# Optimization experiments

Measured on AMD Instinct MI355X. Metric: run time of the kernel, lower is better.

The kernel has to match this reference:

```python
import jax, jax.numpy as jnp
import numpy as np

N = 20000      # nodes
L = 64         # seq_length
E = 64         # emb_size
V = 30000      # vocab_size
HG = 128       # gnn_hidden_size
HT = 128       # text_hidden_size
NE = 640000    # edges
EPS = 1e-12


def _normalize(x):
    # F.normalize(x, p=2, dim=1) on [N, E, L]
    n = jnp.sqrt(jnp.sum(x * x, axis=1, keepdims=True))
    return x / jnp.maximum(n, EPS)


def gcn_conv(x, W, b, src_idx, dst_idx, n_nodes):
    # PyG GCNConv: add self-loops, symmetric normalization D^-1/2 (A+I) D^-1/2 (X W) + b
    h = x @ W                                            # [N, out]
    deg = jnp.zeros((n_nodes,), h.dtype).at[dst_idx].add(1.0) + 1.0  # incl. self-loop
    dinv = jax.lax.rsqrt(deg)
    norm = dinv[src_idx] * dinv[dst_idx]                 # [NE]
    msg = h[src_idx] * norm[:, None]                     # gather + scale
    out = jnp.zeros_like(h).at[dst_idx].add(msg)         # scatter-add to targets
    out = out + h * (dinv * dinv)[:, None]               # self-loop term
    return out + b


def setup_inputs() -> dict:
    key = jax.random.key(0)
    ks = jax.random.split(key, 12)
    rn = lambda k, shape: jax.random.normal(k, shape, jnp.float32) * 0.02
    return {
        "src": jax.random.randint(ks[0], (N, L), 0, V),
        "seg": jax.random.randint(ks[1], (N, L), 0, 3),
        "edge_index": jax.random.randint(ks[2], (2, NE), 0, N),
        "src_emb": rn(ks[3], (V, E)),
        "seg_emb": rn(ks[4], (3, E)),
        "w": jnp.ones((L,), jnp.float32),
        "Wq1": rn(ks[5], (E, HT)), "bq1": jnp.zeros((HT,), jnp.float32),
        "Wq2": rn(ks[6], (HT, E)), "bq2": jnp.zeros((E,), jnp.float32),
        "Wg1": rn(ks[7], (E, HG)), "bg1": jnp.zeros((HG,), jnp.float32),
        "Wg2": rn(ks[8], (HG, E)), "bg2": jnp.zeros((E,), jnp.float32),
        "Wl": rn(ks[9], (E, E)),   "bl": jnp.zeros((E,), jnp.float32),
    }


def reference(src, seg, edge_index, src_emb, seg_emb, w, Wq1, bq1, Wq2, bq2,
              Wg1, bg1, Wg2, bg2, Wl, bl):
    # --- LiteratureEmbedding ---
    se = src_emb[src]                 # [N, L, E]
    ge = seg_emb[seg]                 # [N, L, E]
    sv = se.reshape(-1, E, L)         # raw view (matches torch .view, not transpose)
    gv = ge.reshape(-1, E, L)
    f = (_normalize(w * sv) + _normalize(gv)).sum(-1)   # [N, E]
    # --- query MLP ---
    x = jax.nn.relu(f @ Wq1 + bq1) @ Wq2 + bq2
    # --- two GCN layers ---
    si, di = edge_index[0], edge_index[1]
    x = jax.nn.relu(gcn_conv(x, Wg1, bg1, si, di, N))
    x = jax.nn.relu(gcn_conv(x, Wg2, bg2, si, di, N))
    # --- output linear (dropout is identity in eval) ---
    return x @ Wl + bl
```

## Files before the change

### kernel.cpp

```cpp
#include <hip/hip_runtime.h>

#if defined(__has_builtin)
#if __has_builtin(__builtin_amdgcn_readlane)
#define READLANE(v, l) __builtin_amdgcn_readlane((v), (l))
#else
#define READLANE(v, l) __shfl((v), (l))
#endif
#else
#define READLANE(v, l) __shfl((v), (l))
#endif
__device__ __forceinline__ float readlane_f(float v, int l) {
    return __uint_as_float(READLANE(__float_as_uint(v), l));
}

__device__ __forceinline__ unsigned short f2bf(float x) {
    unsigned u = __float_as_uint(x);
    u += 0x7FFFu + ((u >> 16) & 1u);
    return (unsigned short)(u >> 16);
}

#define CAPLOG 8

__global__ __launch_bounds__(256) void prep0_k(
    const float* __restrict__ src_emb, unsigned short* __restrict__ sbf, int ve,
    int* __restrict__ cursor, int n,
    unsigned* __restrict__ Cz, unsigned* __restrict__ Az, int convB)
{
    const int b = blockIdx.x, t = threadIdx.x;
    if (b < convB) {
        int i = (b * 256 + t) * 4;
        if (i + 3 < ve) {
            float4 v = *(const float4*)&src_emb[i];
            ushort4 u;
            u.x = f2bf(v.x); u.y = f2bf(v.y); u.z = f2bf(v.z); u.w = f2bf(v.w);
            *(ushort4*)&sbf[i] = u;
        } else {
            for (; i < ve; ++i) sbf[i] = f2bf(src_emb[i]);
        }
    } else {
        int i = (b - convB) * 256 + t;
        if (i < n) cursor[i] = 0;
        if (b == convB && t < 32) { Cz[t] = 0u; Az[t] = 0u; }
    }
}

__global__ __launch_bounds__(256) void prep1_k(
    const int* __restrict__ si, const int* __restrict__ di,
    int* __restrict__ cursor, int* __restrict__ edge_off, int ne, int eB,
    const int* __restrict__ src, const int* __restrict__ seg,
    const unsigned short* __restrict__ sbf, const float* __restrict__ seg_emb,
    const float* __restrict__ wvec, float* __restrict__ f)
{
    const int t = threadIdx.x;
    if ((int)blockIdx.x < eB) {
        int i = blockIdx.x * 256 + t;
        if (i < ne) {
            int d = di[i];
            int pos = atomicAdd(cursor + d, 1);
            edge_off[((long)d << CAPLOG) + pos] = si[i] << 7;
        }
        return;
    }
    __shared__ __align__(16) float S[64 * 65];
    __shared__ float red[4][64];
    __shared__ float part2[4][64];
    __shared__ float coef[64];
    __shared__ float rGs[64];
    __shared__ float segE[192];
    __shared__ float dG[3];
    __shared__ int   gidxS[64];
    __shared__ int   cnt3[3];

    const int wid = t >> 6, q = t & 63;
    const long n = blockIdx.x - eB;

    if (wid == 0) {
        int c = seg[n * 64 + q];
        gidxS[q] = c;
        unsigned long long b0 = __ballot(c == 0);
        unsigned long long b1 = __ballot(c == 1);
        if (q == 0) {
            int n0 = __popcll(b0), n1 = __popcll(b1);
            cnt3[0] = n0; cnt3[1] = n1; cnt3[2] = 64 - n0 - n1;
        }
    } else if (t < 64 + 192) {
        segE[t - 64] = seg_emb[t - 64];
    }

    const int p0 = wid * 16;
    int off = src[n * 64 + p0 + (q & 15)] << 7;
    const char* base = (const char*)sbf;
    const int q2 = q << 1;
    float s2 = 0.f;
    #pragma unroll
    for (int pp = 0; pp < 16; ++pp) {
        int so = READLANE(off, pp);
        unsigned short u = *(const unsigned short*)(base + (so + q2));
        float v = __uint_as_float((unsigned)u << 16);
        S[(p0 + pp) * 65 + q] = v;
        s2 += v * v;
    }
    red[wid][q] = s2;
    __syncthreads();

    if (t < 64) {
        float ts = red[0][t] + red[1][t] + red[2][t] + red[3][t];
        float wq = wvec[t];
        coef[t] = wq / fmaxf(fabsf(wq) * sqrtf(ts), 1e-12f);
        float e0 = segE[t], e1 = segE[64 + t], e2 = segE[128 + t];
        float g2 = (float)cnt3[0] * e0 * e0 + (float)cnt3[1] * e1 * e1
                 + (float)cnt3[2] * e2 * e2;
        rGs[t] = 1.f / fmaxf(sqrtf(g2), 1e-12f);
    }
    __syncthreads();

    if (t < 3) {
        float a = 0.f;
        for (int k = 0; k < 64; ++k) a += segE[t * 64 + k] * rGs[k];
        dG[t] = a;
    }
    float acc = 0.f;
    const int k0 = wid * 16;
    #pragma unroll
    for (int kk = 0; kk < 16; ++kk)
        acc += S[q * 65 + k0 + kk] * coef[k0 + kk];
    part2[wid][q] = acc;
    __syncthreads();

    if (t < 64)
        f[n * 64 + t] = part2[0][t] + part2[1][t] + part2[2][t] + part2[3][t]
                        + dG[gidxS[t]];
}

__device__ __forceinline__ float4 csr_gather4_bf(const char* __restrict__ hb,
                                                 const int* __restrict__ eo,
                                                 int dn, int j, int zoff)
{
    const int grp = j >> 4;
    const int col = (j & 15) << 3;
    float4 a0 = make_float4(0.f, 0.f, 0.f, 0.f);
    float4 a1 = a0, a2 = a0, a3 = a0;
#define ACC(d, a)                                                        \
    { a.x += __uint_as_float((d).x << 16);                               \
      a.y += __uint_as_float((d).x & 0xFFFF0000u);                       \
      a.z += __uint_as_float((d).y << 16);                               \
      a.w += __uint_as_float((d).y & 0xFFFF0000u); }
    for (int e = 0; e < dn; e += 64) {
        const int cnt = min(dn - e, 64);
        const int eoff = (e + j < dn) ? eo[e + j] : zoff;
        int m = 0;
        for (; m + 16 <= cnt; m += 16) {
            int o0 = __shfl(eoff, m + grp);
            int o1 = __shfl(eoff, m + 4 + grp);
            int o2 = __shfl(eoff, m + 8 + grp);
            int o3 = __shfl(eoff, m + 12 + grp);
            uint2 d0 = *(const uint2*)(hb + (o0 + col));
            uint2 d1 = *(const uint2*)(hb + (o1 + col));
            uint2 d2 = *(const uint2*)(hb + (o2 + col));
            uint2 d3 = *(const uint2*)(hb + (o3 + col));
            ACC(d0, a0); ACC(d1, a1); ACC(d2, a2); ACC(d3, a3);
        }
        for (; m < cnt; m += 4) {
            int o = __shfl(eoff, m + grp);
            uint2 d = *(const uint2*)(hb + (o + col));
            ACC(d, a0);
        }
    }
#undef ACC
    a0.x += a1.x + a2.x + a3.x;
    a0.y += a1.y + a2.y + a3.y;
    a0.z += a1.z + a2.z + a3.z;
    a0.w += a1.w + a2.w + a3.w;
    a0.x += __shfl_xor(a0.x, 16); a0.x += __shfl_xor(a0.x, 32);
    a0.y += __shfl_xor(a0.y, 16); a0.y += __shfl_xor(a0.y, 32);
    a0.z += __shfl_xor(a0.z, 16); a0.z += __shfl_xor(a0.z, 32);
    a0.w += __shfl_xor(a0.w, 16); a0.w += __shfl_xor(a0.w, 32);
    return a0;
}

__device__ __forceinline__ float4 bf_row4(const char* hb, long rowoff, int col) {
    uint2 d = *(const uint2*)(hb + rowoff + col);
    float4 v;
    v.x = __uint_as_float(d.x << 16);
    v.y = __uint_as_float(d.x & 0xFFFF0000u);
    v.z = __uint_as_float(d.y << 16);
    v.w = __uint_as_float(d.y & 0xFFFF0000u);
    return v;
}

template <bool S2_BIAS>
__device__ __forceinline__ void dense_pair_body(
    float* Wh, float* F, float* H,
    const float* __restrict__ W1, const float* __restrict__ b1,
    const float* __restrict__ W2, const float* __restrict__ b2,
    const int* __restrict__ deg, unsigned short* __restrict__ out,
    int row0, int nrows, int t)
{
    for (int i = t * 4; i < 32 * 128; i += 1024)
        *(float4*)&Wh[i] = *(const float4*)&W1[i];
    __syncthreads();

    const int jg = t & 31, rslot = t >> 5;
    const int j0 = jg * 4;
    float4 acc0, acc1;
    {
        float4 b4 = *(const float4*)&b1[j0];
        acc0 = b4; acc1 = b4;
    }
    #pragma unroll 2
    for (int k = 0; k < 32; k += 4) {
        float4 w0 = *(float4*)&Wh[(k + 0) * 128 + j0];
        float4 w1 = *(float4*)&Wh[(k + 1) * 128 + j0];
        float4 w2 = *(float4*)&Wh[(k + 2) * 128 + j0];
        float4 w3 = *(float4*)&Wh[(k + 3) * 128 + j0];
        float4 fa = *(float4*)&F[rslot * 64 + k];
        float4 fb = *(float4*)&F[(rslot + 8) * 64 + k];
        acc0.x += fa.x * w0.x + fa.y * w1.x + fa.z * w2.x + fa.w * w3.x;
        acc0.y += fa.x * w0.y + fa.y * w1.y + fa.z * w2.y + fa.w * w3.y;
        acc0.z += fa.x * w0.z + fa.y * w1.z + fa.z * w2.z + fa.w * w3.z;
        acc0.w += fa.x * w0.w + fa.y * w1.w + fa.z * w2.w + fa.w * w3.w;
        acc1.x += fb.x * w0.x + fb.y * w1.x + fb.z * w2.x + fb.w * w3.x;
        acc1.y += fb.x * w0.y + fb.y * w1.y + fb.z * w2.y + fb.w * w3.y;
        acc1.z += fb.x * w0.z + fb.y * w1.z + fb.z * w2.z + fb.w * w3.z;
        acc1.w += fb.x * w0.w + fb.y * w1.w + fb.z * w2.w + fb.w * w3.w;
    }
    __syncthreads();
    for (int i = t * 4; i < 32 * 128; i += 1024)
        *(float4*)&Wh[i] = *(const float4*)&W1[32 * 128 + i];
    __syncthreads();
    #pragma unroll 2
    for (int k = 0; k < 32; k += 4) {
        float4 w0 = *(float4*)&Wh[(k + 0) * 128 + j0];
        float4 w1 = *(float4*)&Wh[(k + 1) * 128 + j0];
        float4 w2 = *(float4*)&Wh[(k + 2) * 128 + j0];
        float4 w3 = *(float4*)&Wh[(k + 3) * 128 + j0];
        float4 fa = *(float4*)&F[rslot * 64 + 32 + k];
        float4 fb = *(float4*)&F[(rslot + 8) * 64 + 32 + k];
        acc0.x += fa.x * w0.x + fa.y * w1.x + fa.z * w2.x + fa.w * w3.x;
        acc0.y += fa.x * w0.y + fa.y * w1.y + fa.z * w2.y + fa.w * w3.y;
        acc0.z += fa.x * w0.z + fa.y * w1.z + fa.z * w2.z + fa.w * w3.z;
        acc0.w += fa.x * w0.w + fa.y * w1.w + fa.z * w2.w + fa.w * w3.w;
        acc1.x += fb.x * w0.x + fb.y * w1.x + fb.z * w2.x + fb.w * w3.x;
        acc1.y += fb.x * w0.y + fb.y * w1.y + fb.z * w2.y + fb.w * w3.y;
        acc1.z += fb.x * w0.z + fb.y * w1.z + fb.z * w2.z + fb.w * w3.z;
        acc1.w += fb.x * w0.w + fb.y * w1.w + fb.z * w2.w + fb.w * w3.w;
    }
    {
        float4 v;
        v.x = fmaxf(acc0.x, 0.f); v.y = fmaxf(acc0.y, 0.f);
        v.z = fmaxf(acc0.z, 0.f); v.w = fmaxf(acc0.w, 0.f);
        *(float4*)&H[rslot * 128 + j0] = v;
        v.x = fmaxf(acc1.x, 0.f); v.y = fmaxf(acc1.y, 0.f);
        v.z = fmaxf(acc1.z, 0.f); v.w = fmaxf(acc1.w, 0.f);
        *(float4*)&H[(rslot + 8) * 128 + j0] = v;
    }
    __syncthreads();

    for (int i = t * 4; i < 64 * 64; i += 1024)
        *(float4*)&Wh[i] = *(const float4*)&W2[i];
    __syncthreads();
    const int jg2 = t & 15, r2 = t >> 4;
    const int j02 = jg2 * 4;
    float4 acc = S2_BIAS ? *(const float4*)&b2[j02]
                         : make_float4(0.f, 0.f, 0.f, 0.f);
    #pragma unroll 2
    for (int k = 0; k < 64; k += 4) {
        float4 w0 = *(float4*)&Wh[(k + 0) * 64 + j02];
        float4 w1 = *(float4*)&Wh[(k + 1) * 64 + j02];
        float4 w2 = *(float4*)&Wh[(k + 2) * 64 + j02];
        float4 w3 = *(float4*)&Wh[(k + 3) * 64 + j02];
        float4 fq = *(float4*)&H[r2 * 128 + k];
        acc.x += fq.x * w0.x + fq.y * w1.x + fq.z * w2.x + fq.w * w3.x;
        acc.y += fq.x * w0.y + fq.y * w1.y + fq.z * w2.y + fq.w * w3.y;
        acc.z += fq.x * w0.z + fq.y * w1.z + fq.z * w2.z + fq.w * w3.z;
        acc.w += fq.x * w0.w + fq.y * w1.w + fq.z * w2.w + fq.w * w3.w;
    }
    __syncthreads();
    for (int i = t * 4; i < 64 * 64; i += 1024)
        *(float4*)&Wh[i] = *(const float4*)&W2[64 * 64 + i];
    __syncthreads();
    #pragma unroll 2
    for (int k = 0; k < 64; k += 4) {
        float4 w0 = *(float4*)&Wh[(k + 0) * 64 + j02];
        float4 w1 = *(float4*)&Wh[(k + 1) * 64 + j02];
        float4 w2 = *(float4*)&Wh[(k + 2) * 64 + j02];
        float4 w3 = *(float4*)&Wh[(k + 3) * 64 + j02];
        float4 fq = *(float4*)&H[r2 * 128 + 64 + k];
        acc.x += fq.x * w0.x + fq.y * w1.x + fq.z * w2.x + fq.w * w3.x;
        acc.y += fq.x * w0.y + fq.y * w1.y + fq.z * w2.y + fq.w * w3.y;
        acc.z += fq.x * w0.z + fq.y * w1.z + fq.z * w2.z + fq.w * w3.z;
        acc.w += fq.x * w0.w + fq.y * w1.w + fq.z * w2.w + fq.w * w3.w;
    }
    const int r = row0 + r2;
    if (r < nrows) {
        float sc = rsqrtf((float)deg[r] + 1.0f);
        ushort4 v;
        v.x = f2bf(acc.x * sc); v.y = f2bf(acc.y * sc);
        v.z = f2bf(acc.z * sc); v.w = f2bf(acc.w * sc);
        *(ushort4*)&out[(long)r * 64 + j02] = v;
    }
}

template <bool S2_BIAS>
__global__ __launch_bounds__(256, 5) void fused2_k(
    const float* __restrict__ in, const float* __restrict__ W1,
    const float* __restrict__ b1, const float* __restrict__ W2,
    const float* __restrict__ b2, const int* __restrict__ deg,
    unsigned short* __restrict__ out, int nrows)
{
    __shared__ __align__(16) float Wh[32 * 128];
    __shared__ __align__(16) float F[16 * 64];
    __shared__ __align__(16) float H[16 * 128];
    const int t = threadIdx.x;
    const int row0 = blockIdx.x * 16;

    for (int i = t * 4; i < 16 * 64; i += 1024) {
        int r = i >> 6;
        float4 v = make_float4(0.f, 0.f, 0.f, 0.f);
        if (row0 + r < nrows) v = *(const float4*)&in[(long)row0 * 64 + i];
        *(float4*)&F[i] = v;
    }
    dense_pair_body<S2_BIAS>(Wh, F, H, W1, b1, W2, b2, deg, out, row0, nrows, t);
}

__global__ __launch_bounds__(256, 5) void gcnfused_k(
    const unsigned short* __restrict__ C, const int* __restrict__ deg,
    const int* __restrict__ edge_off,
    const float* __restrict__ W1, const float* __restrict__ b1,
    const float* __restrict__ W2, unsigned short* __restrict__ out,
    int nrows, int zoff)
{
    __shared__ __align__(16) float Wh[32 * 128];
    __shared__ __align__(16) float F[16 * 64];
    __shared__ __align__(16) float H[16 * 128];
    const int t = threadIdx.x;
    const int row0 = blockIdx.x * 16;
    const int wv = t >> 6, j = t & 63;
    const int col = (j & 15) << 3;

    const char* hb = (const char*)C;
    #pragma unroll
    for (int i = 0; i < 4; ++i) {
        const int r = wv * 4 + i;
        const int node = row0 + r;
        if (node < nrows) {
            float4 agg = csr_gather4_bf(hb, edge_off + ((long)node << CAPLOG),
                                        deg[node], j, zoff);
            float4 self = bf_row4(hb, (long)node << 7, col);
            float dv = rsqrtf((float)deg[node] + 1.0f);
            if ((j >> 4) == 0) {
                float4 res;
                res.x = dv * (self.x + agg.x);
                res.y = dv * (self.y + agg.y);
                res.z = dv * (self.z + agg.z);
                res.w = dv * (self.w + agg.w);
                *(float4*)&F[r * 64 + (j & 15) * 4] = res;
            }
        } else if ((j >> 4) == 0) {
            *(float4*)&F[r * 64 + (j & 15) * 4] = make_float4(0.f, 0.f, 0.f, 0.f);
        }
    }
    dense_pair_body<false>(Wh, F, H, W1, b1, W2, nullptr, deg, out, row0, nrows, t);
}

__global__ __launch_bounds__(256) void gatherout_k(
    const unsigned short* __restrict__ hp, const int* __restrict__ deg,
    const int* __restrict__ edge_off,
    const float* __restrict__ bg2, const float* __restrict__ Wl,
    const float* __restrict__ bl, float* __restrict__ out, int n, int zoff)
{
    __shared__ __align__(16) float WlL[64 * 64];
    __shared__ __align__(16) float vS[4][64];
    const int t = threadIdx.x;
    for (int i = t * 4; i < 64 * 64; i += 1024)
        *(float4*)&WlL[i] = *(const float4*)&Wl[i];
    __syncthreads();

    const int row0 = blockIdx.x * 16;
    const int wv = t >> 6, j = t & 63;
    const int col = (j & 15) << 3;
    const char* hb = (const char*)hp;
    const float blj = bl[j];
    const float4 bg4 = *(const float4*)&bg2[(j & 15) * 4];

    #pragma unroll
    for (int i = 0; i < 4; ++i) {
        const int node = row0 + wv * 4 + i;
        if (node >= n) continue;
        float4 agg = csr_gather4_bf(hb, edge_off + ((long)node << CAPLOG),
                                    deg[node], j, zoff);
        float4 self = bf_row4(hb, (long)node << 7, col);
        const float dv = rsqrtf((float)deg[node] + 1.0f);
        float4 vf;
        vf.x = fmaxf(dv * (self.x + agg.x) + bg4.x, 0.f);
        vf.y = fmaxf(dv * (self.y + agg.y) + bg4.y, 0.f);
        vf.z = fmaxf(dv * (self.z + agg.z) + bg4.z, 0.f);
        vf.w = fmaxf(dv * (self.w + agg.w) + bg4.w, 0.f);
        if ((j >> 4) == 0) *(float4*)&vS[wv][(j & 15) * 4] = vf;
        const float v = vS[wv][j];

        float o = blj;
        #pragma unroll 4
        for (int k = 0; k < 64; k += 4) {
            float vk0 = readlane_f(v, k + 0);
            float vk1 = readlane_f(v, k + 1);
            float vk2 = readlane_f(v, k + 2);
            float vk3 = readlane_f(v, k + 3);
            o += vk0 * WlL[(k + 0) * 64 + j] + vk1 * WlL[(k + 1) * 64 + j]
               + vk2 * WlL[(k + 2) * 64 + j] + vk3 * WlL[(k + 3) * 64 + j];
        }
        out[(long)node * 64 + j] = o;
    }
}

extern "C" void kernel_launch(void* const* d_in, const int* in_sizes, int n_in,
                              void* d_out, int out_size, void* d_ws, size_t ws_size,
                              hipStream_t stream) {
    const int*   src     = (const int*)  d_in[0];
    const int*   seg     = (const int*)  d_in[1];
    const int*   ei      = (const int*)  d_in[2];
    const float* src_emb = (const float*)d_in[3];
    const float* seg_emb = (const float*)d_in[4];
    const float* w       = (const float*)d_in[5];
    const float* Wq1     = (const float*)d_in[6];
    const float* bq1     = (const float*)d_in[7];
    const float* Wq2     = (const float*)d_in[8];
    const float* bq2     = (const float*)d_in[9];
    const float* Wg1     = (const float*)d_in[10];
    const float* bg1     = (const float*)d_in[11];
    const float* Wg2     = (const float*)d_in[12];
    const float* bg2     = (const float*)d_in[13];
    const float* Wl      = (const float*)d_in[14];
    const float* bl      = (const float*)d_in[15];
    float* out = (float*)d_out;

    const int N  = in_sizes[0] / 64;
    const int NE = in_sizes[2] / 2;
    const int VE = in_sizes[3];
    const int* si = ei;
    const int* di = ei + NE;

    const size_t Npad  = ((size_t)N + 3) & ~(size_t)3;
    const size_t VEpad = ((size_t)VE + 7) & ~(size_t)7;
    int* cursor   = (int*)d_ws;
    int* edge_off = cursor + Npad;
    unsigned short* sbf = (unsigned short*)(edge_off + ((size_t)N << CAPLOG));
    float* A32 = (float*)(sbf + VEpad);
    unsigned short* Cbf = (unsigned short*)(A32 + (size_t)N * 64);
    unsigned short* Abf = Cbf + (size_t)N * 64 + 64;
    const int zoff = N << 7;

    dim3 b256(256);
    const int convB = (VE + 1023) / 1024;
    const int zB    = (N + 255) / 256;
    const int eB    = (NE + 255) / 256;
    const int fB    = (N + 15) / 16;

    prep0_k<<<convB + zB, b256, 0, stream>>>(src_emb, sbf, VE, cursor, N,
                                             (unsigned*)(Cbf + (size_t)N * 64),
                                             (unsigned*)(Abf + (size_t)N * 64),
                                             convB);
    prep1_k<<<eB + N, b256, 0, stream>>>(si, di, cursor, edge_off, NE, eB,
                                         src, seg, sbf, seg_emb, w, A32);

    fused2_k<true><<<fB, b256, 0, stream>>>(A32, Wq1, bq1, Wq2, bq2,
                                            cursor, Cbf, N);

    gcnfused_k<<<fB, b256, 0, stream>>>(Cbf, cursor, edge_off,
                                        Wg1, bg1, Wg2, Abf, N, zoff);

    gatherout_k<<<fB, b256, 0, stream>>>(Abf, cursor, edge_off, bg2,
                                         Wl, bl, out, N, zoff);
}
```

Baseline: 228.1 us.

## Compute literature embedding with one wavefront per node instead of one block

The embedding stage of prep1_k now processes four nodes per 256-thread block, one wavefront each, instead of one node per block. Each lane loads 8-byte bf16 vectors, and the column norms and segment-embedding dot products are reduced with cross-lane shuffles, which removes the block-wide barriers and most shared-memory staging. The bf16 rows are read twice, once for the norms and once for the weighted sum. This cuts the launch to about a quarter of the blocks, at the cost of redundant loads and more shuffle work per lane.

```diff
diff --git a/kernel.cpp b/kernel.cpp
--- a/kernel.cpp
+++ b/kernel.cpp
@@ -49,7 +49,7 @@
     int* __restrict__ cursor, int* __restrict__ edge_off, int ne, int eB,
     const int* __restrict__ src, const int* __restrict__ seg,
     const unsigned short* __restrict__ sbf, const float* __restrict__ seg_emb,
-    const float* __restrict__ wvec, float* __restrict__ f)
+    const float* __restrict__ wvec, float* __restrict__ f, int nN)
 {
     const int t = threadIdx.x;
     if ((int)blockIdx.x < eB) {
@@ -61,75 +61,76 @@
         }
         return;
     }
-    __shared__ __align__(16) float S[64 * 65];
-    __shared__ float red[4][64];
-    __shared__ float part2[4][64];
-    __shared__ float coef[64];
-    __shared__ float rGs[64];
-    __shared__ float segE[192];
-    __shared__ float dG[3];
-    __shared__ int   gidxS[64];
-    __shared__ int   cnt3[3];
+    __shared__ __align__(16) float coefS[4][64];
+    __shared__ float scr[4][16 * 66];
 
     const int wid = t >> 6, q = t & 63;
-    const long n = blockIdx.x - eB;
-
-    if (wid == 0) {
-        int c = seg[n * 64 + q];
-        gidxS[q] = c;
-        unsigned long long b0 = __ballot(c == 0);
-        unsigned long long b1 = __ballot(c == 1);
-        if (q == 0) {
-            int n0 = __popcll(b0), n1 = __popcll(b1);
-            cnt3[0] = n0; cnt3[1] = n1; cnt3[2] = 64 - n0 - n1;
-        }
-    } else if (t < 64 + 192) {
-        segE[t - 64] = seg_emb[t - 64];
-    }
-
-    const int p0 = wid * 16;
-    int off = src[n * 64 + p0 + (q & 15)] << 7;
+    const long n = ((long)blockIdx.x - eB) * 4 + wid;
+    if (n >= nN) return;
+    const int grp = q >> 4, c = q & 15;
+
+    const int off = src[n * 64 + q] << 7;
+    const int sg  = seg[n * 64 + q];
+    const float e0 = seg_emb[q], e1 = seg_emb[64 + q], e2 = seg_emb[128 + q];
     const char* base = (const char*)sbf;
-    const int q2 = q << 1;
-    float s2 = 0.f;
+
+    float t0 = 0.f, t1 = 0.f, t2 = 0.f, t3 = 0.f;
+    #pragma unroll 8
+    for (int i = 0; i < 16; ++i) {
+        int ro = __shfl(off, i * 4 + grp);
+        uint2 d = *(const uint2*)(base + (ro + c * 8));
+        float v0 = __uint_as_float(d.x << 16);
+        float v1 = __uint_as_float(d.x & 0xFFFF0000u);
+        float v2 = __uint_as_float(d.y << 16);
+        float v3 = __uint_as_float(d.y & 0xFFFF0000u);
+        t0 += v0 * v0; t1 += v1 * v1; t2 += v2 * v2; t3 += v3 * v3;
+    }
+    t0 += __shfl_xor(t0, 16); t0 += __shfl_xor(t0, 32);
+    t1 += __shfl_xor(t1, 16); t1 += __shfl_xor(t1, 32);
+    t2 += __shfl_xor(t2, 16); t2 += __shfl_xor(t2, 32);
+    t3 += __shfl_xor(t3, 16); t3 += __shfl_xor(t3, 32);
+
+    const float4 wv = *(const float4*)&wvec[c * 4];
+    float4 cf;
+    cf.x = wv.x / fmaxf(fabsf(wv.x) * sqrtf(t0), 1e-12f);
+    cf.y = wv.y / fmaxf(fabsf(wv.y) * sqrtf(t1), 1e-12f);
+    cf.z = wv.z / fmaxf(fabsf(wv.z) * sqrtf(t2), 1e-12f);
+    cf.w = wv.w / fmaxf(fabsf(wv.w) * sqrtf(t3), 1e-12f);
+    if (grp == 0) *(float4*)&coefS[wid][c * 4] = cf;
+
+    unsigned long long b0 = __ballot(sg == 0);
+    unsigned long long b1 = __ballot(sg == 1);
+    float n0 = (float)__popcll(b0), n1 = (float)__popcll(b1);
+    float n2 = 64.f - n0 - n1;
+    float g2 = n0 * e0 * e0 + n1 * e1 * e1 + n2 * e2 * e2;
+    float rg = 1.f / fmaxf(sqrtf(g2), 1e-12f);
+    float p0 = e0 * rg, p1 = e1 * rg, p2 = e2 * rg;
     #pragma unroll
-    for (int pp = 0; pp < 16; ++pp) {
-        int so = READLANE(off, pp);
-        unsigned short u = *(const unsigned short*)(base + (so + q2));
-        float v = __uint_as_float((unsigned)u << 16);
-        S[(p0 + pp) * 65 + q] = v;
-        s2 += v * v;
-    }
-    red[wid][q] = s2;
-    __syncthreads();
-
-    if (t < 64) {
-        float ts = red[0][t] + red[1][t] + red[2][t] + red[3][t];
-        float wq = wvec[t];
-        coef[t] = wq / fmaxf(fabsf(wq) * sqrtf(ts), 1e-12f);
-        float e0 = segE[t], e1 = segE[64 + t], e2 = segE[128 + t];
-        float g2 = (float)cnt3[0] * e0 * e0 + (float)cnt3[1] * e1 * e1
-                 + (float)cnt3[2] * e2 * e2;
-        rGs[t] = 1.f / fmaxf(sqrtf(g2), 1e-12f);
-    }
-    __syncthreads();
-
-    if (t < 3) {
-        float a = 0.f;
-        for (int k = 0; k < 64; ++k) a += segE[t * 64 + k] * rGs[k];
-        dG[t] = a;
-    }
-    float acc = 0.f;
-    const int k0 = wid * 16;
+    for (int m = 1; m < 64; m <<= 1) {
+        p0 += __shfl_xor(p0, m);
+        p1 += __shfl_xor(p1, m);
+        p2 += __shfl_xor(p2, m);
+    }
+
+    const float4 cfb = *(const float4*)&coefS[wid][c * 4];
+    float* sw = scr[wid];
+    #pragma unroll 8
+    for (int i = 0; i < 16; ++i) {
+        int ro = __shfl(off, i * 4 + grp);
+        uint2 d = *(const uint2*)(base + (ro + c * 8));
+        float po = __uint_as_float(d.x << 16)          * cfb.x
+                 + __uint_as_float(d.x & 0xFFFF0000u)  * cfb.y
+                 + __uint_as_float(d.y << 16)          * cfb.z
+                 + __uint_as_float(d.y & 0xFFFF0000u)  * cfb.w;
+        sw[c * 66 + i * 4 + grp] = po;
+    }
+    float out = 0.f;
     #pragma unroll
-    for (int kk = 0; kk < 16; ++kk)
-        acc += S[q * 65 + k0 + kk] * coef[k0 + kk];
-    part2[wid][q] = acc;
-    __syncthreads();
-
-    if (t < 64)
-        f[n * 64 + t] = part2[0][t] + part2[1][t] + part2[2][t] + part2[3][t]
-                        + dG[gidxS[t]];
+    for (int c2 = 0; c2 < 16; ++c2)
+        out += sw[c2 * 66 + q];
+
+    const float dg = (sg == 0) ? p0 : ((sg == 1) ? p1 : p2);
+    f[n * 64 + q] = out + dg;
 }
 
 __device__ __forceinline__ float4 csr_gather4_bf(const char* __restrict__ hb,
@@ -454,14 +455,15 @@
     const int convB = (VE + 1023) / 1024;
     const int zB    = (N + 255) / 256;
     const int eB    = (NE + 255) / 256;
+    const int nB    = (N + 3) / 4;
     const int fB    = (N + 15) / 16;
 
     prep0_k<<<convB + zB, b256, 0, stream>>>(src_emb, sbf, VE, cursor, N,
                                              (unsigned*)(Cbf + (size_t)N * 64),
                                              (unsigned*)(Abf + (size_t)N * 64),
                                              convB);
-    prep1_k<<<eB + N, b256, 0, stream>>>(si, di, cursor, edge_off, NE, eB,
-                                         src, seg, sbf, seg_emb, w, A32);
+    prep1_k<<<eB + nB, b256, 0, stream>>>(si, di, cursor, edge_off, NE, eB,
+                                          src, seg, sbf, seg_emb, w, A32, N);
 
     fused2_k<true><<<fB, b256, 0, stream>>>(A32, Wq1, bq1, Wq2, bq2,
                                             cursor, Cbf, N);
```

Result: faster. 222.1 us (-2.6%).
